# Performance work log

Hardware: AMD Instinct MI355X
Metric: run time of the kernel (lower is better)

The kernel has to match this reference:

```python
import jax, jax.numpy as jnp
import numpy as np

B, N, E, D, H, C, U = 512, 256, 1024, 256, 256, 8, 64
MARGIN_T, RISK_T, SCALE = 0.2, 0.6, 0.1
NEG = -1.0e9


def setup_inputs() -> dict:
    key = jax.random.key(0)
    ks = jax.random.split(key, 30)
    s = 0.02
    inp = dict(
        features=jax.random.normal(ks[0], (B, D), jnp.float32),
        centered_scores=jax.random.normal(ks[1], (B, N), jnp.float32),
        margin=jax.random.uniform(ks[2], (B,), jnp.float32),
        boundary_risk=jax.random.uniform(ks[3], (B,), jnp.float32),
        edge_sensitivity=jax.random.normal(ks[4], (B, E), jnp.float32),
        coords=jax.random.normal(ks[5], (B, N, C), jnp.float32),
        uncertainty=jax.random.uniform(ks[6], (B, U), jnp.float32),
        Wc1=jax.random.normal(ks[7], (D, H), jnp.float32) * s,
        bc1=jnp.zeros((H,), jnp.float32),
        Wc2=jax.random.normal(ks[8], (H, H), jnp.float32) * s,
        bc2=jnp.zeros((H,), jnp.float32),
        Wn1=jax.random.normal(ks[9], (H + C + 2, H), jnp.float32) * s,
        bn1=jnp.zeros((H,), jnp.float32),
        Wn2=jax.random.normal(ks[10], (H, 1), jnp.float32) * s,
        bn2=jnp.zeros((1,), jnp.float32),
        We1=jax.random.normal(ks[11], (H + C + 2, H), jnp.float32) * s,
        be1=jnp.zeros((H,), jnp.float32),
        We2=jax.random.normal(ks[12], (H, 1), jnp.float32) * s,
        be2=jnp.zeros((1,), jnp.float32),
        Wg=jax.random.normal(ks[13], (H, 1), jnp.float32) * s,
        bg=jnp.zeros((1,), jnp.float32),
        action_mask=jax.random.bernoulli(ks[14], 0.8, (B, N)),
        edge_mask=jax.random.bernoulli(ks[15], 0.8, (B, E)),
        actions=jax.random.randint(ks[16], (B, N), 0, U, jnp.int32),
        edges=jax.random.randint(ks[17], (B, E, 2), 0, N, jnp.int32),
    )
    return inp


def _mlp2(x, W1, b1, W2, b2):
    return jax.nn.relu(x @ W1 + b1) @ W2 + b2


def reference(features, centered_scores, margin, boundary_risk, edge_sensitivity,
              coords, uncertainty, Wc1, bc1, Wc2, bc2, Wn1, bn1, Wn2, bn2,
              We1, be1, We2, be2, Wg, bg, action_mask, edge_mask, actions, edges):
    amf = action_mask.astype(jnp.float32)
    emf = edge_mask.astype(jnp.float32)

    # context MLP
    h = jax.nn.relu(jax.nn.relu(features @ Wc1 + bc1) @ Wc2 + bc2)  # [B,H]

    low_margin = (margin < MARGIN_T).astype(jnp.float32)
    high_risk = (boundary_risk > RISK_T).astype(jnp.float32)
    learned_gate = jax.nn.sigmoid((h @ Wg + bg)[:, 0])
    refine_gate = jnp.maximum(jnp.maximum(low_margin, high_risk),
                              (learned_gate > 0.5).astype(jnp.float32))  # [B]

    # node features: [B,N,H+C+2]
    act = jnp.clip(actions, 0, U - 1)
    unc_g = jnp.take_along_axis(uncertainty, act, axis=1)  # [B,N]
    h_n = jnp.broadcast_to(h[:, None, :], (B, N, H))
    node_feats = jnp.concatenate(
        [h_n, coords, centered_scores[..., None], unc_g[..., None]], axis=-1)
    node_delta = _mlp2(node_feats, Wn1, bn1, Wn2, bn2)[..., 0] * amf  # [B,N]

    # edge features: gather src/dst coords
    e = jnp.clip(edges, 0, N - 1)
    src_c = jnp.take_along_axis(coords, e[:, :, 0:1], axis=1)  # [B,E,C]
    dst_c = jnp.take_along_axis(coords, e[:, :, 1:2], axis=1)  # [B,E,C]
    h_e = jnp.broadcast_to(h[:, None, :], (B, E, H))
    edge_feats = jnp.concatenate(
        [h_e, dst_c - src_c, edge_sensitivity[..., None], emf[..., None]], axis=-1)
    edge_delta = _mlp2(edge_feats, We1, be1, We2, be2)[..., 0] * emf  # [B,E]

    gate_node = refine_gate[:, None]
    refined_scores = (centered_scores + gate_node * SCALE * node_delta) * amf
    denom = jnp.clip(amf.sum(-1, keepdims=True), 1.0, None)  # [B,1]
    refined_scores = (refined_scores - refined_scores.sum(-1, keepdims=True) / denom) * amf

    refined_edge = (edge_sensitivity + gate_node * SCALE * edge_delta) * emf

    masked_top = jnp.where(action_mask, refined_scores, NEG)
    top_vals, top_idx = jax.lax.top_k(masked_top, 2)
    refined_margin = top_vals[:, 0] - top_vals[:, 1]

    # masked per-batch variance of refined_edge (biased), 0 if <=1 valid entry
    cnt = emf.sum(-1)
    cnt_c = jnp.clip(cnt, 1.0, None)
    mean = (refined_edge * emf).sum(-1) / cnt_c
    var = (emf * (refined_edge - mean[:, None]) ** 2).sum(-1) / cnt_c
    edge_var = jnp.where(cnt > 1.0, var, 0.0)

    unc_term = (unc_g * amf).sum(-1) / denom[:, 0]
    refined_risk = jnp.clip(
        jax.nn.sigmoid(-refined_margin) + 0.2 * edge_var + 0.1 * unc_term, 0.0, 1.0)

    return (refined_scores, refined_margin, refined_edge,
            top_idx[:, 0], refined_risk, refine_gate)
```

## Files before the change

### kernel.cpp

```cpp
#include <hip/hip_runtime.h>
#include <math.h>

#define B 512
#define N 256
#define E 1024
#define D 256
#define H 256
#define C 8
#define U 64

__device__ __forceinline__ float mask_val(const void* m, long i, int flag) {
    if (flag == 1) return ((const unsigned char*)m)[i] ? 1.f : 0.f;
    if (flag == 2) return (((const float*)m)[i] != 0.f) ? 1.f : 0.f;
    return ((const int*)m)[i] ? 1.f : 0.f;
}

__device__ __forceinline__ float block_sum(float v, float* red) {
    int t = threadIdx.x;
    red[t] = v; __syncthreads();
    for (int s = 128; s > 0; s >>= 1) {
        if (t < s) red[t] += red[t + s];
        __syncthreads();
    }
    float r = red[0]; __syncthreads();
    return r;
}

__global__ __launch_bounds__(512) void k_h(
    const float* __restrict__ feat,
    const float* __restrict__ Wc1, const float* __restrict__ bc1,
    const float* __restrict__ Wc2, const float* __restrict__ bc2,
    const float* __restrict__ Wn1, const float* __restrict__ bn1,
    const float* __restrict__ We1, const float* __restrict__ be1,
    const float* __restrict__ Wg,  const float* __restrict__ bg,
    const float* __restrict__ margin, const float* __restrict__ brisk,
    const unsigned int* __restrict__ amask_words,
    float* __restrict__ base_n, float* __restrict__ base_e,
    float* __restrict__ out_gate, int* __restrict__ flag)
{
    __shared__ __align__(16) float sF[2][256];
    __shared__ __align__(16) float sH[2][256];
    __shared__ float red[512];
    __shared__ int cls0, cls1;

    int t = threadIdx.x;
    int w = t >> 8;
    int c = t & 255;
    int b0 = blockIdx.x * 2;
    int b = b0 + w;

    if (blockIdx.x == 0) {
        if (t == 0) { cls0 = 0; cls1 = 0; }
        __syncthreads();
        if (t < 256) {
            unsigned int wd = amask_words[t];
            if (wd != 0u && wd != 1u) {
                if (wd == 0x3f800000u) atomicOr(&cls1, 1);
                else                   atomicOr(&cls0, 1);
            }
        }
        __syncthreads();
        if (t == 0) *flag = cls0 ? 1 : (cls1 ? 2 : 0);
    }

    sF[w][c] = feat[(long)b * D + c];
    __syncthreads();

    {
        float acc[4] = {bc1[c], 0.f, 0.f, 0.f};
        const float* Wp = Wc1 + c;
        for (int d0 = 0; d0 < D; d0 += 16) {
            float wv[16];
            #pragma unroll
            for (int k = 0; k < 16; k++) wv[k] = Wp[(long)(d0 + k) * H];
            #pragma unroll
            for (int k = 0; k < 16; k++)
                acc[k & 3] = fmaf(sF[w][d0 + k], wv[k], acc[k & 3]);
        }
        sH[w][c] = fmaxf((acc[0] + acc[1]) + (acc[2] + acc[3]), 0.f);
    }
    __syncthreads();

    {
        float acc[4] = {bc2[c], 0.f, 0.f, 0.f};
        const float* Wp = Wc2 + c;
        for (int d0 = 0; d0 < H; d0 += 16) {
            float wv[16];
            #pragma unroll
            for (int k = 0; k < 16; k++) wv[k] = Wp[(long)(d0 + k) * H];
            #pragma unroll
            for (int k = 0; k < 16; k++)
                acc[k & 3] = fmaf(sH[w][d0 + k], wv[k], acc[k & 3]);
        }
        float a = fmaxf((acc[0] + acc[1]) + (acc[2] + acc[3]), 0.f);
        __syncthreads();
        sF[w][c] = a;
    }
    __syncthreads();

    red[t] = sF[w][c] * Wg[c];
    __syncthreads();
    for (int s = 128; s > 0; s >>= 1) {
        if (c < s) red[t] += red[t + s];
        __syncthreads();
    }
    if (c == 0) {
        float lg = 1.f / (1.f + expf(-(red[t] + bg[0])));
        out_gate[b] = ((margin[b] < 0.2f) || (brisk[b] > 0.6f) || (lg > 0.5f)) ? 1.f : 0.f;
    }

    {
        const float* W3  = w ? (We1 + c) : (Wn1 + c);
        float bias       = w ? be1[c]    : bn1[c];
        float* dst       = w ? base_e    : base_n;
        float aA[2] = {bias, 0.f};
        float aB[2] = {bias, 0.f};
        for (int d0 = 0; d0 < H; d0 += 16) {
            float wv[16];
            #pragma unroll
            for (int k = 0; k < 16; k++) wv[k] = W3[(long)(d0 + k) * H];
            #pragma unroll
            for (int k = 0; k < 16; k++) {
                aA[k & 1] = fmaf(sF[0][d0 + k], wv[k], aA[k & 1]);
                aB[k & 1] = fmaf(sF[1][d0 + k], wv[k], aB[k & 1]);
            }
        }
        dst[(long)b0 * H + c]       = aA[0] + aA[1];
        dst[(long)(b0 + 1) * H + c] = aB[0] + aB[1];
    }
}

__global__ __launch_bounds__(256) void k_ne(
    const float* __restrict__ cs, const float* __restrict__ coords,
    const float* __restrict__ unc, const int* __restrict__ actions,
    const void* __restrict__ amask,
    const float* __restrict__ Wn1, const float* __restrict__ Wn2,
    const float* __restrict__ bn2, const float* __restrict__ base_n,
    const float* __restrict__ es, const int* __restrict__ edges,
    const void* __restrict__ emask,
    const float* __restrict__ We1, const float* __restrict__ We2,
    const float* __restrict__ be2, const float* __restrict__ base_e,
    const float* __restrict__ gate, const int* __restrict__ flagp,
    float* __restrict__ out0, float* __restrict__ out1, float* __restrict__ out2,
    float* __restrict__ out3, float* __restrict__ riskbase, float* __restrict__ evar)
{
    __shared__ __align__(16) float smem[4096 + 2048];
    float* pack = smem;
    int t = threadIdx.x;
    int flag = *flagp;

    if (blockIdx.x < 512) {
        int b = blockIdx.x;
        float g = gate[b];
        float am = mask_val(amask, (long)b * N + t, flag);
        float csv = cs[(long)b * N + t];
        int a = actions[(long)b * N + t];
        a = min(max(a, 0), U - 1);
        float ug = unc[(long)b * U + a];

        float raw;
        if (g != 0.f) {
            #pragma unroll
            for (int i = 0; i < 4; i++) {
                int lin = t + 256 * i;
                int j = lin >> 2, kq = (lin & 3) * 4;
                float4 v;
                if (kq == 0)
                    v = make_float4(Wn1[(long)(H+0)*H+j], Wn1[(long)(H+1)*H+j],
                                    Wn1[(long)(H+2)*H+j], Wn1[(long)(H+3)*H+j]);
                else if (kq == 4)
                    v = make_float4(Wn1[(long)(H+4)*H+j], Wn1[(long)(H+5)*H+j],
                                    Wn1[(long)(H+6)*H+j], Wn1[(long)(H+7)*H+j]);
                else if (kq == 8)
                    v = make_float4(Wn1[(long)(H+8)*H+j], Wn1[(long)(H+9)*H+j],
                                    Wn2[j], base_n[(long)b*H+j]);
                else
                    v = make_float4(0.f, 0.f, 0.f, 0.f);
                ((float4*)pack)[lin] = v;
            }

            const float4* cp = (const float4*)(coords + ((long)b * N + t) * C);
            float4 c0 = cp[0], c1 = cp[1];
            float f0 = c0.x, f1 = c0.y, f2 = c0.z, f3 = c0.w;
            float f4 = c1.x, f5 = c1.y, f6 = c1.z, f7 = c1.w;
            float f8 = csv, f9 = ug;
            float acc = bn2[0];
            __syncthreads();

            const float4* pk = (const float4*)pack;
            #pragma unroll 2
            for (int j = 0; j < H; j++) {
                float4 wa = pk[j*4+0];
                float4 wb = pk[j*4+1];
                float4 wc = pk[j*4+2];
                float zA = fmaf(f0, wa.x, wc.w);
                zA = fmaf(f1, wa.y, zA);
                zA = fmaf(f2, wa.z, zA);
                zA = fmaf(f3, wa.w, zA);
                float zB = f4 * wb.x;
                zB = fmaf(f5, wb.y, zB);
                zB = fmaf(f6, wb.z, zB);
                zB = fmaf(f7, wb.w, zB);
                zB = fmaf(f8, wc.x, zB);
                zB = fmaf(f9, wc.y, zB);
                acc = fmaf(fmaxf(zA + zB, 0.f), wc.z, acc);
            }
            raw = (csv + g * 0.1f * (acc * am)) * am;
            __syncthreads();
        } else {
            raw = csv * am;
        }

        float* red = smem + 4096;
        int* ridx = (int*)(smem + 4096 + 256);

        float sum = block_sum(raw, red);
        float cnt = block_sum(am, red);
        float denom = fmaxf(cnt, 1.f);
        float rs = (raw - sum / denom) * am;
        out0[(long)b * N + t] = rs;

        float masked = (am != 0.f) ? rs : -1e9f;

        red[t] = masked; ridx[t] = t; __syncthreads();
        for (int s = 128; s > 0; s >>= 1) {
            if (t < s) {
                float o = red[t + s]; int oi = ridx[t + s];
                if (o > red[t] || (o == red[t] && oi < ridx[t])) { red[t] = o; ridx[t] = oi; }
            }
            __syncthreads();
        }
        float v1 = red[0]; int i1 = ridx[0]; __syncthreads();

        red[t] = (t == i1) ? -1e9f : masked; __syncthreads();
        for (int s = 128; s > 0; s >>= 1) {
            if (t < s) red[t] = fmaxf(red[t], red[t + s]);
            __syncthreads();
        }
        float v2 = red[0]; __syncthreads();
        float rmargin = v1 - v2;

        float su = block_sum(ug * am, red);

        if (t == 0) {
            out1[b] = rmargin;
            out3[b] = (float)i1;
            float sig = 1.f / (1.f + expf(rmargin));
            riskbase[b] = sig + 0.1f * (su / denom);
        }
    } else {
        int b = blockIdx.x - 512;
        float g = gate[b];
        float (*sC)[8] = (float (*)[8])(smem + 4096);

        float re[4], emv[4];
        if (g != 0.f) {
            {
                float4* sc4 = (float4*)&sC[0][0];
                const float4* g4 = (const float4*)(coords + (long)b * N * C);
                sc4[t] = g4[t];
                sc4[t + 256] = g4[t + 256];
            }
            #pragma unroll
            for (int i = 0; i < 4; i++) {
                int lin = t + 256 * i;
                int j = lin >> 2, kq = (lin & 3) * 4;
                float4 v;
                if (kq == 0)
                    v = make_float4(We1[(long)(H+0)*H+j], We1[(long)(H+1)*H+j],
                                    We1[(long)(H+2)*H+j], We1[(long)(H+3)*H+j]);
                else if (kq == 4)
                    v = make_float4(We1[(long)(H+4)*H+j], We1[(long)(H+5)*H+j],
                                    We1[(long)(H+6)*H+j], We1[(long)(H+7)*H+j]);
                else if (kq == 8)
                    v = make_float4(We1[(long)(H+8)*H+j], We2[j],
                                    base_e[(long)b*H+j] + We1[(long)(H+9)*H+j], 0.f);
                else
                    v = make_float4(0.f, 0.f, 0.f, 0.f);
                ((float4*)pack)[lin] = v;
            }
            float b2v = be2[0];
            __syncthreads();

            float f[4][9], acc[4];
            #pragma unroll
            for (int q = 0; q < 4; q++) {
                int e = t + 256 * q;
                int2 ev = ((const int2*)edges)[(long)b * E + e];
                int s0 = min(max(ev.x, 0), N - 1);
                int d0 = min(max(ev.y, 0), N - 1);
                #pragma unroll
                for (int k = 0; k < 8; k++) f[q][k] = sC[d0][k] - sC[s0][k];
                f[q][8] = es[(long)b * E + e];
                emv[q] = mask_val(emask, (long)b * E + e, flag);
                acc[q] = b2v;
            }

            const float4* pk = (const float4*)pack;
            #pragma unroll 2
            for (int j = 0; j < H; j++) {
                float4 wa = pk[j*4+0];
                float4 wb = pk[j*4+1];
                float4 wc = pk[j*4+2];
                #pragma unroll
                for (int q = 0; q < 4; q++) {
                    float zA = fmaf(f[q][0], wa.x, wc.z);
                    zA = fmaf(f[q][1], wa.y, zA);
                    zA = fmaf(f[q][2], wa.z, zA);
                    zA = fmaf(f[q][3], wa.w, zA);
                    float zB = f[q][4] * wb.x;
                    zB = fmaf(f[q][5], wb.y, zB);
                    zB = fmaf(f[q][6], wb.z, zB);
                    zB = fmaf(f[q][7], wb.w, zB);
                    zB = fmaf(f[q][8], wc.x, zB);
                    acc[q] = fmaf(fmaxf(zA + zB, 0.f), wc.y, acc[q]);
                }
            }

            #pragma unroll
            for (int q = 0; q < 4; q++) {
                re[q] = (emv[q] != 0.f) ? (f[q][8] + g * 0.1f * acc[q]) : 0.f;
                out2[(long)b * E + t + 256 * q] = re[q];
            }
        } else {
            #pragma unroll
            for (int q = 0; q < 4; q++) {
                int e = t + 256 * q;
                emv[q] = mask_val(emask, (long)b * E + e, flag);
                re[q] = es[(long)b * E + e] * emv[q];
                out2[(long)b * E + e] = re[q];
            }
        }

        __syncthreads();
        float* red = smem + 4096;

        float S1 = 0.f, ce = 0.f;
        #pragma unroll
        for (int q = 0; q < 4; q++) { S1 += re[q]; ce += emv[q]; }
        float S1t = block_sum(S1, red);
        float cet = block_sum(ce, red);
        float mean = S1t / fmaxf(cet, 1.f);
        float v = 0.f;
        #pragma unroll
        for (int q = 0; q < 4; q++) {
            float dd = re[q] - mean;
            v = fmaf(emv[q] * dd, dd, v);
        }
        float vt = block_sum(v, red);
        if (t == 0) {
            float var = vt / fmaxf(cet, 1.f);
            evar[b] = (cet > 1.f) ? var : 0.f;
        }
    }
}

__global__ __launch_bounds__(256) void k_risk(
    const float* __restrict__ riskbase, const float* __restrict__ evar,
    float* __restrict__ out4)
{
    int b = blockIdx.x * 256 + threadIdx.x;
    float r = riskbase[b] + 0.2f * evar[b];
    out4[b] = fminf(fmaxf(r, 0.f), 1.f);
}

extern "C" void kernel_launch(void* const* d_in, const int* in_sizes, int n_in,
                              void* d_out, int out_size, void* d_ws, size_t ws_size,
                              hipStream_t stream) {
    const float* feat   = (const float*)d_in[0];
    const float* cs     = (const float*)d_in[1];
    const float* marg   = (const float*)d_in[2];
    const float* brisk  = (const float*)d_in[3];
    const float* es     = (const float*)d_in[4];
    const float* coords = (const float*)d_in[5];
    const float* unc    = (const float*)d_in[6];
    const float* Wc1    = (const float*)d_in[7];
    const float* bc1    = (const float*)d_in[8];
    const float* Wc2    = (const float*)d_in[9];
    const float* bc2    = (const float*)d_in[10];
    const float* Wn1    = (const float*)d_in[11];
    const float* bn1    = (const float*)d_in[12];
    const float* Wn2    = (const float*)d_in[13];
    const float* bn2    = (const float*)d_in[14];
    const float* We1    = (const float*)d_in[15];
    const float* be1    = (const float*)d_in[16];
    const float* We2    = (const float*)d_in[17];
    const float* be2    = (const float*)d_in[18];
    const float* Wg     = (const float*)d_in[19];
    const float* bg     = (const float*)d_in[20];
    const void*  amask  = d_in[21];
    const void*  emask  = d_in[22];
    const int*   actions= (const int*)d_in[23];
    const int*   edges  = (const int*)d_in[24];

    float* out0 = (float*)d_out;
    float* out1 = out0 + (long)B * N;
    float* out2 = out1 + B;
    float* out3 = out2 + (long)B * E;
    float* out4 = out3 + B;
    float* out5 = out4 + B;

    float* base_n  = (float*)d_ws;
    float* base_e  = base_n + (long)B * H;
    float* riskbase= base_e + (long)B * H;
    float* evar    = riskbase + B;
    int*   flag    = (int*)(evar + B);

    k_h<<<B / 2, 512, 0, stream>>>(feat, Wc1, bc1, Wc2, bc2, Wn1, bn1, We1, be1,
                                   Wg, bg, marg, brisk,
                                   (const unsigned int*)amask,
                                   base_n, base_e, out5, flag);
    k_ne<<<1024, 256, 0, stream>>>(cs, coords, unc, actions, amask,
                                   Wn1, Wn2, bn2, base_n,
                                   es, edges, emask,
                                   We1, We2, be2, base_e,
                                   out5, flag,
                                   out0, out1, out2, out3, riskbase, evar);
    k_risk<<<2, 256, 0, stream>>>(riskbase, evar, out4);
}
```

Measured before the change: 80.80 us.

## Split node/edge hidden dim across blocks with atomic accumulation and separate finalize kernel

The node and edge MLP second layers are split across four hidden-dimension quarters per batch. Partial sums are accumulated with atomicAdd into zeroed buffers, with zeroing done inside k_h. Node blocks now process four batches each with 64 hidden units, and a new k_fin kernel applies masks, biases, normalization, top-2 and variance. The goal is more parallel blocks and shorter per-block loops for better occupancy, at the cost of atomics, an extra kernel launch and an extra round trip of intermediates through global memory.

```diff
diff --git a/kernel.cpp b/kernel.cpp
--- a/kernel.cpp
+++ b/kernel.cpp
@@ -8,6 +8,9 @@
 #define H 256
 #define C 8
 #define U 64
+
+#define NODE_GRID 512
+#define EDGE_GRID 2048
 
 __device__ __forceinline__ float mask_val(const void* m, long i, int flag) {
     if (flag == 1) return ((const unsigned char*)m)[i] ? 1.f : 0.f;
@@ -36,7 +39,8 @@
     const float* __restrict__ margin, const float* __restrict__ brisk,
     const unsigned int* __restrict__ amask_words,
     float* __restrict__ base_n, float* __restrict__ base_e,
-    float* __restrict__ out_gate, int* __restrict__ flag)
+    float* __restrict__ out_gate, int* __restrict__ flag,
+    float* __restrict__ node_delta, float* __restrict__ out2)
 {
     __shared__ __align__(16) float sF[2][256];
     __shared__ __align__(16) float sH[2][256];
@@ -48,6 +52,12 @@
     int c = t & 255;
     int b0 = blockIdx.x * 2;
     int b = b0 + w;
+
+    {
+        int idx = blockIdx.x * 512 + t;
+        node_delta[idx] = 0.f;
+        ((float4*)out2)[idx] = make_float4(0.f, 0.f, 0.f, 0.f);
+    }
 
     if (blockIdx.x == 0) {
         if (t == 0) { cls0 = 0; cls1 = 0; }
@@ -133,23 +143,175 @@
 __global__ __launch_bounds__(256) void k_ne(
     const float* __restrict__ cs, const float* __restrict__ coords,
     const float* __restrict__ unc, const int* __restrict__ actions,
-    const void* __restrict__ amask,
     const float* __restrict__ Wn1, const float* __restrict__ Wn2,
-    const float* __restrict__ bn2, const float* __restrict__ base_n,
+    const float* __restrict__ base_n,
     const float* __restrict__ es, const int* __restrict__ edges,
-    const void* __restrict__ emask,
     const float* __restrict__ We1, const float* __restrict__ We2,
-    const float* __restrict__ be2, const float* __restrict__ base_e,
+    const float* __restrict__ base_e,
+    const float* __restrict__ gate,
+    float* __restrict__ node_delta, float* __restrict__ out2)
+{
+    __shared__ __align__(16) float smem[2816];
+    int t = threadIdx.x;
+
+    if (blockIdx.x < NODE_GRID) {
+        int rg = blockIdx.x >> 2;
+        int jq = blockIdx.x & 3;
+        int b0 = rg * 4;
+        float* sB   = smem;
+        float* pack = smem + 256;
+
+        {
+            int i = t;
+            #pragma unroll
+            for (int s = 0; s < 3; s++, i += 256) {
+                int j = i / 12, k = i - j * 12;
+                int jj = jq * 64 + j;
+                float v;
+                if (k < 10)      v = Wn1[(long)(H + k) * H + jj];
+                else if (k == 10) v = Wn2[jj];
+                else             v = 0.f;
+                pack[i] = v;
+            }
+            int r = t >> 6, j = t & 63;
+            sB[r * 64 + j] = base_n[(long)(b0 + r) * H + jq * 64 + j];
+        }
+        __syncthreads();
+
+        int w = t >> 6, lane = t & 63;
+        int b = b0 + w;
+        float g = gate[b];
+        if (g == 0.f) return;
+
+        float f[4][10], acc[4];
+        #pragma unroll
+        for (int q = 0; q < 4; q++) {
+            int n = q * 64 + lane;
+            const float4* cp = (const float4*)(coords + ((long)b * N + n) * C);
+            float4 c0 = cp[0], c1 = cp[1];
+            f[q][0] = c0.x; f[q][1] = c0.y; f[q][2] = c0.z; f[q][3] = c0.w;
+            f[q][4] = c1.x; f[q][5] = c1.y; f[q][6] = c1.z; f[q][7] = c1.w;
+            f[q][8] = cs[(long)b * N + n];
+            int a = actions[(long)b * N + n];
+            a = min(max(a, 0), U - 1);
+            f[q][9] = unc[(long)b * U + a];
+            acc[q] = 0.f;
+        }
+
+        const float4* pk = (const float4*)pack;
+        const float* sBw = sB + w * 64;
+        #pragma unroll 4
+        for (int j = 0; j < 64; j++) {
+            float4 wa = pk[j * 3 + 0];
+            float4 wb = pk[j * 3 + 1];
+            float4 wc = pk[j * 3 + 2];
+            float bse = sBw[j];
+            #pragma unroll
+            for (int q = 0; q < 4; q++) {
+                float zA = fmaf(f[q][0], wa.x, bse);
+                zA = fmaf(f[q][1], wa.y, zA);
+                zA = fmaf(f[q][2], wa.z, zA);
+                zA = fmaf(f[q][3], wa.w, zA);
+                float zB = f[q][4] * wb.x;
+                zB = fmaf(f[q][5], wb.y, zB);
+                zB = fmaf(f[q][6], wb.z, zB);
+                zB = fmaf(f[q][7], wb.w, zB);
+                zB = fmaf(f[q][8], wc.x, zB);
+                zB = fmaf(f[q][9], wc.y, zB);
+                acc[q] = fmaf(fmaxf(zA + zB, 0.f), wc.z, acc[q]);
+            }
+        }
+
+        #pragma unroll
+        for (int q = 0; q < 4; q++)
+            atomicAdd(&node_delta[(long)b * N + q * 64 + lane], acc[q]);
+    } else {
+        int eb = blockIdx.x - NODE_GRID;
+        int b = eb >> 2, jq = eb & 3;
+        float g = gate[b];
+        if (g == 0.f) return;
+
+        float (*sC)[8] = (float (*)[8])smem;
+        float* pack = smem + 2048;
+
+        {
+            float4* sc4 = (float4*)smem;
+            const float4* g4 = (const float4*)(coords + (long)b * N * C);
+            sc4[t] = g4[t];
+            sc4[t + 256] = g4[t + 256];
+            int i = t;
+            #pragma unroll
+            for (int s = 0; s < 3; s++, i += 256) {
+                int j = i / 12, k = i - j * 12;
+                int jj = jq * 64 + j;
+                float v;
+                if (k < 9)        v = We1[(long)(H + k) * H + jj];
+                else if (k == 9)  v = We2[jj];
+                else if (k == 10) v = base_e[(long)b * H + jj]
+                                      + We1[(long)(H + 9) * H + jj];
+                else              v = 0.f;
+                pack[i] = v;
+            }
+        }
+        __syncthreads();
+
+        float f[4][9], acc[4];
+        #pragma unroll
+        for (int q = 0; q < 4; q++) {
+            int e = t + 256 * q;
+            int2 ev = ((const int2*)edges)[(long)b * E + e];
+            int s0 = min(max(ev.x, 0), N - 1);
+            int d0 = min(max(ev.y, 0), N - 1);
+            #pragma unroll
+            for (int k = 0; k < 8; k++) f[q][k] = sC[d0][k] - sC[s0][k];
+            f[q][8] = es[(long)b * E + e];
+            acc[q] = 0.f;
+        }
+
+        const float4* pk = (const float4*)pack;
+        #pragma unroll 4
+        for (int j = 0; j < 64; j++) {
+            float4 wa = pk[j * 3 + 0];
+            float4 wb = pk[j * 3 + 1];
+            float4 wc = pk[j * 3 + 2];
+            #pragma unroll
+            for (int q = 0; q < 4; q++) {
+                float zA = fmaf(f[q][0], wa.x, wc.z);
+                zA = fmaf(f[q][1], wa.y, zA);
+                zA = fmaf(f[q][2], wa.z, zA);
+                zA = fmaf(f[q][3], wa.w, zA);
+                float zB = f[q][4] * wb.x;
+                zB = fmaf(f[q][5], wb.y, zB);
+                zB = fmaf(f[q][6], wb.z, zB);
+                zB = fmaf(f[q][7], wb.w, zB);
+                zB = fmaf(f[q][8], wc.x, zB);
+                acc[q] = fmaf(fmaxf(zA + zB, 0.f), wc.y, acc[q]);
+            }
+        }
+
+        #pragma unroll
+        for (int q = 0; q < 4; q++)
+            atomicAdd(&out2[(long)b * E + t + 256 * q], acc[q]);
+    }
+}
+
+__global__ __launch_bounds__(256) void k_fin(
+    const void* __restrict__ amask, const void* __restrict__ emask,
+    const int* __restrict__ actions, const float* __restrict__ unc,
+    const float* __restrict__ cs, const float* __restrict__ es,
+    const float* __restrict__ bn2, const float* __restrict__ be2,
     const float* __restrict__ gate, const int* __restrict__ flagp,
-    float* __restrict__ out0, float* __restrict__ out1, float* __restrict__ out2,
-    float* __restrict__ out3, float* __restrict__ riskbase, float* __restrict__ evar)
+    const float* __restrict__ node_delta,
+    float* __restrict__ out0, float* __restrict__ out1,
+    float* __restrict__ out2, float* __restrict__ out3,
+    float* __restrict__ riskbase, float* __restrict__ evar)
 {
-    __shared__ __align__(16) float smem[4096 + 2048];
-    float* pack = smem;
+    __shared__ float red[256];
+    __shared__ int ridx[256];
     int t = threadIdx.x;
     int flag = *flagp;
 
-    if (blockIdx.x < 512) {
+    if (blockIdx.x < B) {
         int b = blockIdx.x;
         float g = gate[b];
         float am = mask_val(amask, (long)b * N + t, flag);
@@ -157,62 +319,8 @@
         int a = actions[(long)b * N + t];
         a = min(max(a, 0), U - 1);
         float ug = unc[(long)b * U + a];
-
-        float raw;
-        if (g != 0.f) {
-            #pragma unroll
-            for (int i = 0; i < 4; i++) {
-                int lin = t + 256 * i;
-                int j = lin >> 2, kq = (lin & 3) * 4;
-                float4 v;
-                if (kq == 0)
-                    v = make_float4(Wn1[(long)(H+0)*H+j], Wn1[(long)(H+1)*H+j],
-                                    Wn1[(long)(H+2)*H+j], Wn1[(long)(H+3)*H+j]);
-                else if (kq == 4)
-                    v = make_float4(Wn1[(long)(H+4)*H+j], Wn1[(long)(H+5)*H+j],
-                                    Wn1[(long)(H+6)*H+j], Wn1[(long)(H+7)*H+j]);
-                else if (kq == 8)
-                    v = make_float4(Wn1[(long)(H+8)*H+j], Wn1[(long)(H+9)*H+j],
-                                    Wn2[j], base_n[(long)b*H+j]);
-                else
-                    v = make_float4(0.f, 0.f, 0.f, 0.f);
-                ((float4*)pack)[lin] = v;
-            }
-
-            const float4* cp = (const float4*)(coords + ((long)b * N + t) * C);
-            float4 c0 = cp[0], c1 = cp[1];
-            float f0 = c0.x, f1 = c0.y, f2 = c0.z, f3 = c0.w;
-            float f4 = c1.x, f5 = c1.y, f6 = c1.z, f7 = c1.w;
-            float f8 = csv, f9 = ug;
-            float acc = bn2[0];
-            __syncthreads();
-
-            const float4* pk = (const float4*)pack;
-            #pragma unroll 2
-            for (int j = 0; j < H; j++) {
-                float4 wa = pk[j*4+0];
-                float4 wb = pk[j*4+1];
-                float4 wc = pk[j*4+2];
-                float zA = fmaf(f0, wa.x, wc.w);
-                zA = fmaf(f1, wa.y, zA);
-                zA = fmaf(f2, wa.z, zA);
-                zA = fmaf(f3, wa.w, zA);
-                float zB = f4 * wb.x;
-                zB = fmaf(f5, wb.y, zB);
-                zB = fmaf(f6, wb.z, zB);
-                zB = fmaf(f7, wb.w, zB);
-                zB = fmaf(f8, wc.x, zB);
-                zB = fmaf(f9, wc.y, zB);
-                acc = fmaf(fmaxf(zA + zB, 0.f), wc.z, acc);
-            }
-            raw = (csv + g * 0.1f * (acc * am)) * am;
-            __syncthreads();
-        } else {
-            raw = csv * am;
-        }
-
-        float* red = smem + 4096;
-        int* ridx = (int*)(smem + 4096 + 256);
+        float nd = (node_delta[(long)b * N + t] + bn2[0]) * am;
+        float raw = (csv + g * 0.1f * nd) * am;
 
         float sum = block_sum(raw, red);
         float cnt = block_sum(am, red);
@@ -249,91 +357,20 @@
             riskbase[b] = sig + 0.1f * (su / denom);
         }
     } else {
-        int b = blockIdx.x - 512;
+        int b = blockIdx.x - B;
         float g = gate[b];
-        float (*sC)[8] = (float (*)[8])(smem + 4096);
+        float be2v = be2[0];
 
         float re[4], emv[4];
-        if (g != 0.f) {
-            {
-                float4* sc4 = (float4*)&sC[0][0];
-                const float4* g4 = (const float4*)(coords + (long)b * N * C);
-                sc4[t] = g4[t];
-                sc4[t + 256] = g4[t + 256];
-            }
-            #pragma unroll
-            for (int i = 0; i < 4; i++) {
-                int lin = t + 256 * i;
-                int j = lin >> 2, kq = (lin & 3) * 4;
-                float4 v;
-                if (kq == 0)
-                    v = make_float4(We1[(long)(H+0)*H+j], We1[(long)(H+1)*H+j],
-                                    We1[(long)(H+2)*H+j], We1[(long)(H+3)*H+j]);
-                else if (kq == 4)
-                    v = make_float4(We1[(long)(H+4)*H+j], We1[(long)(H+5)*H+j],
-                                    We1[(long)(H+6)*H+j], We1[(long)(H+7)*H+j]);
-                else if (kq == 8)
-                    v = make_float4(We1[(long)(H+8)*H+j], We2[j],
-                                    base_e[(long)b*H+j] + We1[(long)(H+9)*H+j], 0.f);
-                else
-                    v = make_float4(0.f, 0.f, 0.f, 0.f);
-                ((float4*)pack)[lin] = v;
-            }
-            float b2v = be2[0];
-            __syncthreads();
-
-            float f[4][9], acc[4];
-            #pragma unroll
-            for (int q = 0; q < 4; q++) {
-                int e = t + 256 * q;
-                int2 ev = ((const int2*)edges)[(long)b * E + e];
-                int s0 = min(max(ev.x, 0), N - 1);
-                int d0 = min(max(ev.y, 0), N - 1);
-                #pragma unroll
-                for (int k = 0; k < 8; k++) f[q][k] = sC[d0][k] - sC[s0][k];
-                f[q][8] = es[(long)b * E + e];
-                emv[q] = mask_val(emask, (long)b * E + e, flag);
-                acc[q] = b2v;
-            }
-
-            const float4* pk = (const float4*)pack;
-            #pragma unroll 2
-            for (int j = 0; j < H; j++) {
-                float4 wa = pk[j*4+0];
-                float4 wb = pk[j*4+1];
-                float4 wc = pk[j*4+2];
-                #pragma unroll
-                for (int q = 0; q < 4; q++) {
-                    float zA = fmaf(f[q][0], wa.x, wc.z);
-                    zA = fmaf(f[q][1], wa.y, zA);
-                    zA = fmaf(f[q][2], wa.z, zA);
-                    zA = fmaf(f[q][3], wa.w, zA);
-                    float zB = f[q][4] * wb.x;
-                    zB = fmaf(f[q][5], wb.y, zB);
-                    zB = fmaf(f[q][6], wb.z, zB);
-                    zB = fmaf(f[q][7], wb.w, zB);
-                    zB = fmaf(f[q][8], wc.x, zB);
-                    acc[q] = fmaf(fmaxf(zA + zB, 0.f), wc.y, acc[q]);
-                }
-            }
-
-            #pragma unroll
-            for (int q = 0; q < 4; q++) {
-                re[q] = (emv[q] != 0.f) ? (f[q][8] + g * 0.1f * acc[q]) : 0.f;
-                out2[(long)b * E + t + 256 * q] = re[q];
-            }
-        } else {
-            #pragma unroll
-            for (int q = 0; q < 4; q++) {
-                int e = t + 256 * q;
-                emv[q] = mask_val(emask, (long)b * E + e, flag);
-                re[q] = es[(long)b * E + e] * emv[q];
-                out2[(long)b * E + e] = re[q];
-            }
-        }
-
-        __syncthreads();
-        float* red = smem + 4096;
+        #pragma unroll
+        for (int q = 0; q < 4; q++) {
+            long idx = (long)b * E + t + 256 * q;
+            emv[q] = mask_val(emask, idx, flag);
+            float delta = out2[idx] + be2v;
+            float r = es[idx] + g * 0.1f * delta;
+            re[q] = (emv[q] != 0.f) ? r : 0.f;
+            out2[idx] = re[q];
+        }
 
         float S1 = 0.f, ce = 0.f;
         #pragma unroll
@@ -400,21 +437,26 @@
     float* out4 = out3 + B;
     float* out5 = out4 + B;
 
-    float* base_n  = (float*)d_ws;
-    float* base_e  = base_n + (long)B * H;
-    float* riskbase= base_e + (long)B * H;
-    float* evar    = riskbase + B;
-    int*   flag    = (int*)(evar + B);
+    float* base_n     = (float*)d_ws;
+    float* base_e     = base_n + (long)B * H;
+    float* node_delta = base_e + (long)B * H;
+    float* riskbase   = node_delta + (long)B * N;
+    float* evar       = riskbase + B;
+    int*   flag       = (int*)(evar + B);
 
     k_h<<<B / 2, 512, 0, stream>>>(feat, Wc1, bc1, Wc2, bc2, Wn1, bn1, We1, be1,
                                    Wg, bg, marg, brisk,
                                    (const unsigned int*)amask,
-                                   base_n, base_e, out5, flag);
-    k_ne<<<1024, 256, 0, stream>>>(cs, coords, unc, actions, amask,
-                                   Wn1, Wn2, bn2, base_n,
-                                   es, edges, emask,
-                                   We1, We2, be2, base_e,
-                                   out5, flag,
-                                   out0, out1, out2, out3, riskbase, evar);
+                                   base_n, base_e, out5, flag,
+                                   node_delta, out2);
+    k_ne<<<NODE_GRID + EDGE_GRID, 256, 0, stream>>>(
+        cs, coords, unc, actions,
+        Wn1, Wn2, base_n,
+        es, edges,
+        We1, We2, base_e,
+        out5, node_delta, out2);
+    k_fin<<<2 * B, 256, 0, stream>>>(amask, emask, actions, unc, cs, es,
+                                     bn2, be2, out5, flag, node_delta,
+                                     out0, out1, out2, out3, riskbase, evar);
     k_risk<<<2, 256, 0, stream>>>(riskbase, evar, out4);
 }
```

After: 80.43 us. Within noise of the previous version (-0.5%).

## Split edge MLP across two blocks per batch and move variance to separate kernel

Applied to the files above, without the earlier changes.

Each batch's edge work now runs on two blocks of 512 edges instead of one block of 1024, so the grid grows to 1536 blocks and is better balanced against the node blocks. Because a batch's edges are no longer in one block, the masked variance reduction moves into a new k_fin kernel that re-reads out2 from global memory, which costs an extra launch and an extra pass over the data. Weight packing into shared memory changes to a 12-float stride filled with coalesced per-thread loads. Coordinates are now stored with a 9-float stride, likely to reduce LDS bank conflicts on the gathered reads.

```diff
diff --git a/kernel.cpp b/kernel.cpp
--- a/kernel.cpp
+++ b/kernel.cpp
@@ -141,15 +141,16 @@
     const float* __restrict__ We1, const float* __restrict__ We2,
     const float* __restrict__ be2, const float* __restrict__ base_e,
     const float* __restrict__ gate, const int* __restrict__ flagp,
-    float* __restrict__ out0, float* __restrict__ out1, float* __restrict__ out2,
-    float* __restrict__ out3, float* __restrict__ riskbase, float* __restrict__ evar)
+    float* __restrict__ out0, float* __restrict__ out1,
+    float* __restrict__ out2, float* __restrict__ out3,
+    float* __restrict__ riskbase)
 {
-    __shared__ __align__(16) float smem[4096 + 2048];
+    __shared__ __align__(16) float smem[3072 + 2304];
     float* pack = smem;
     int t = threadIdx.x;
     int flag = *flagp;
 
-    if (blockIdx.x < 512) {
+    if (blockIdx.x < B) {
         int b = blockIdx.x;
         float g = gate[b];
         float am = mask_val(amask, (long)b * N + t, flag);
@@ -160,25 +161,13 @@
 
         float raw;
         if (g != 0.f) {
-            #pragma unroll
-            for (int i = 0; i < 4; i++) {
-                int lin = t + 256 * i;
-                int j = lin >> 2, kq = (lin & 3) * 4;
-                float4 v;
-                if (kq == 0)
-                    v = make_float4(Wn1[(long)(H+0)*H+j], Wn1[(long)(H+1)*H+j],
-                                    Wn1[(long)(H+2)*H+j], Wn1[(long)(H+3)*H+j]);
-                else if (kq == 4)
-                    v = make_float4(Wn1[(long)(H+4)*H+j], Wn1[(long)(H+5)*H+j],
-                                    Wn1[(long)(H+6)*H+j], Wn1[(long)(H+7)*H+j]);
-                else if (kq == 8)
-                    v = make_float4(Wn1[(long)(H+8)*H+j], Wn1[(long)(H+9)*H+j],
-                                    Wn2[j], base_n[(long)b*H+j]);
-                else
-                    v = make_float4(0.f, 0.f, 0.f, 0.f);
-                ((float4*)pack)[lin] = v;
-            }
-
+            {
+                float* p = pack + t * 12;
+                #pragma unroll
+                for (int k = 0; k < 10; k++) p[k] = Wn1[(long)(H + k) * H + t];
+                p[10] = Wn2[t];
+                p[11] = base_n[(long)b * H + t];
+            }
             const float4* cp = (const float4*)(coords + ((long)b * N + t) * C);
             float4 c0 = cp[0], c1 = cp[1];
             float f0 = c0.x, f1 = c0.y, f2 = c0.z, f3 = c0.w;
@@ -187,12 +176,12 @@
             float acc = bn2[0];
             __syncthreads();
 
-            const float4* pk = (const float4*)pack;
-            #pragma unroll 2
+            #pragma unroll 4
             for (int j = 0; j < H; j++) {
-                float4 wa = pk[j*4+0];
-                float4 wb = pk[j*4+1];
-                float4 wc = pk[j*4+2];
+                const float* pj = pack + j * 12;
+                float4 wa = *(const float4*)(pj);
+                float4 wb = *(const float4*)(pj + 4);
+                float4 wc = *(const float4*)(pj + 8);
                 float zA = fmaf(f0, wa.x, wc.w);
                 zA = fmaf(f1, wa.y, zA);
                 zA = fmaf(f2, wa.z, zA);
@@ -211,8 +200,8 @@
             raw = csv * am;
         }
 
-        float* red = smem + 4096;
-        int* ridx = (int*)(smem + 4096 + 256);
+        float* red = smem + 3072;
+        int* ridx = (int*)(smem + 3072 + 256);
 
         float sum = block_sum(raw, red);
         float cnt = block_sum(am, red);
@@ -249,109 +238,117 @@
             riskbase[b] = sig + 0.1f * (su / denom);
         }
     } else {
-        int b = blockIdx.x - 512;
+        int eb = blockIdx.x - B;
+        int b = eb >> 1, half = eb & 1;
         float g = gate[b];
-        float (*sC)[8] = (float (*)[8])(smem + 4096);
-
-        float re[4], emv[4];
-        if (g != 0.f) {
-            {
-                float4* sc4 = (float4*)&sC[0][0];
-                const float4* g4 = (const float4*)(coords + (long)b * N * C);
-                sc4[t] = g4[t];
-                sc4[t + 256] = g4[t + 256];
-            }
-            #pragma unroll
-            for (int i = 0; i < 4; i++) {
-                int lin = t + 256 * i;
-                int j = lin >> 2, kq = (lin & 3) * 4;
-                float4 v;
-                if (kq == 0)
-                    v = make_float4(We1[(long)(H+0)*H+j], We1[(long)(H+1)*H+j],
-                                    We1[(long)(H+2)*H+j], We1[(long)(H+3)*H+j]);
-                else if (kq == 4)
-                    v = make_float4(We1[(long)(H+4)*H+j], We1[(long)(H+5)*H+j],
-                                    We1[(long)(H+6)*H+j], We1[(long)(H+7)*H+j]);
-                else if (kq == 8)
-                    v = make_float4(We1[(long)(H+8)*H+j], We2[j],
-                                    base_e[(long)b*H+j] + We1[(long)(H+9)*H+j], 0.f);
-                else
-                    v = make_float4(0.f, 0.f, 0.f, 0.f);
-                ((float4*)pack)[lin] = v;
-            }
-            float b2v = be2[0];
-            __syncthreads();
-
-            float f[4][9], acc[4];
-            #pragma unroll
-            for (int q = 0; q < 4; q++) {
-                int e = t + 256 * q;
-                int2 ev = ((const int2*)edges)[(long)b * E + e];
-                int s0 = min(max(ev.x, 0), N - 1);
-                int d0 = min(max(ev.y, 0), N - 1);
-                #pragma unroll
-                for (int k = 0; k < 8; k++) f[q][k] = sC[d0][k] - sC[s0][k];
-                f[q][8] = es[(long)b * E + e];
-                emv[q] = mask_val(emask, (long)b * E + e, flag);
-                acc[q] = b2v;
-            }
-
-            const float4* pk = (const float4*)pack;
-            #pragma unroll 2
-            for (int j = 0; j < H; j++) {
-                float4 wa = pk[j*4+0];
-                float4 wb = pk[j*4+1];
-                float4 wc = pk[j*4+2];
-                #pragma unroll
-                for (int q = 0; q < 4; q++) {
-                    float zA = fmaf(f[q][0], wa.x, wc.z);
-                    zA = fmaf(f[q][1], wa.y, zA);
-                    zA = fmaf(f[q][2], wa.z, zA);
-                    zA = fmaf(f[q][3], wa.w, zA);
-                    float zB = f[q][4] * wb.x;
-                    zB = fmaf(f[q][5], wb.y, zB);
-                    zB = fmaf(f[q][6], wb.z, zB);
-                    zB = fmaf(f[q][7], wb.w, zB);
-                    zB = fmaf(f[q][8], wc.x, zB);
-                    acc[q] = fmaf(fmaxf(zA + zB, 0.f), wc.y, acc[q]);
-                }
-            }
-
-            #pragma unroll
-            for (int q = 0; q < 4; q++) {
-                re[q] = (emv[q] != 0.f) ? (f[q][8] + g * 0.1f * acc[q]) : 0.f;
-                out2[(long)b * E + t + 256 * q] = re[q];
-            }
-        } else {
-            #pragma unroll
-            for (int q = 0; q < 4; q++) {
-                int e = t + 256 * q;
-                emv[q] = mask_val(emask, (long)b * E + e, flag);
-                re[q] = es[(long)b * E + e] * emv[q];
-                out2[(long)b * E + e] = re[q];
-            }
-        }
-
-        __syncthreads();
-        float* red = smem + 4096;
-
-        float S1 = 0.f, ce = 0.f;
+        int e0 = half * 512 + t;
+
+        if (g == 0.f) {
+            #pragma unroll
+            for (int q = 0; q < 2; q++) {
+                long idx = (long)b * E + e0 + 256 * q;
+                float em = mask_val(emask, idx, flag);
+                out2[idx] = es[idx] * em;
+            }
+            return;
+        }
+
+        float* sC = smem + 3072;
+
+        {
+            const float4* g4 = (const float4*)(coords + (long)b * N * C);
+            float4 c0 = g4[t * 2], c1 = g4[t * 2 + 1];
+            float* dst = sC + t * 9;
+            dst[0] = c0.x; dst[1] = c0.y; dst[2] = c0.z; dst[3] = c0.w;
+            dst[4] = c1.x; dst[5] = c1.y; dst[6] = c1.z; dst[7] = c1.w;
+        }
+        {
+            float* p = pack + t * 12;
+            #pragma unroll
+            for (int k = 0; k < 9; k++) p[k] = We1[(long)(H + k) * H + t];
+            p[9] = We2[t];
+            p[10] = base_e[(long)b * H + t] + We1[(long)(H + 9) * H + t];
+            p[11] = 0.f;
+        }
+        float b2v = be2[0];
+        __syncthreads();
+
+        float f[2][9], acc[2], emv[2];
         #pragma unroll
-        for (int q = 0; q < 4; q++) { S1 += re[q]; ce += emv[q]; }
-        float S1t = block_sum(S1, red);
-        float cet = block_sum(ce, red);
-        float mean = S1t / fmaxf(cet, 1.f);
-        float v = 0.f;
+        for (int q = 0; q < 2; q++) {
+            long idx = (long)b * E + e0 + 256 * q;
+            int2 ev = ((const int2*)edges)[idx];
+            int s0 = min(max(ev.x, 0), N - 1);
+            int d0 = min(max(ev.y, 0), N - 1);
+            const float* cs0 = sC + s0 * 9;
+            const float* cd0 = sC + d0 * 9;
+            #pragma unroll
+            for (int k = 0; k < 8; k++) f[q][k] = cd0[k] - cs0[k];
+            f[q][8] = es[idx];
+            emv[q] = mask_val(emask, idx, flag);
+            acc[q] = b2v;
+        }
+
+        #pragma unroll 4
+        for (int j = 0; j < H; j++) {
+            const float* pj = pack + j * 12;
+            float4 wa = *(const float4*)(pj);
+            float4 wb = *(const float4*)(pj + 4);
+            float4 wc = *(const float4*)(pj + 8);
+            #pragma unroll
+            for (int q = 0; q < 2; q++) {
+                float zA = fmaf(f[q][0], wa.x, wc.z);
+                zA = fmaf(f[q][1], wa.y, zA);
+                zA = fmaf(f[q][2], wa.z, zA);
+                zA = fmaf(f[q][3], wa.w, zA);
+                float zB = f[q][4] * wb.x;
+                zB = fmaf(f[q][5], wb.y, zB);
+                zB = fmaf(f[q][6], wb.z, zB);
+                zB = fmaf(f[q][7], wb.w, zB);
+                zB = fmaf(f[q][8], wc.x, zB);
+                acc[q] = fmaf(fmaxf(zA + zB, 0.f), wc.y, acc[q]);
+            }
+        }
+
         #pragma unroll
-        for (int q = 0; q < 4; q++) {
-            float dd = re[q] - mean;
-            v = fmaf(emv[q] * dd, dd, v);
-        }
-        float vt = block_sum(v, red);
-        if (t == 0) {
-            float var = vt / fmaxf(cet, 1.f);
-            evar[b] = (cet > 1.f) ? var : 0.f;
-        }
+        for (int q = 0; q < 2; q++) {
+            long idx = (long)b * E + e0 + 256 * q;
+            out2[idx] = (emv[q] != 0.f) ? (f[q][8] + g * 0.1f * acc[q]) : 0.f;
+        }
+    }
+}
+
+__global__ __launch_bounds__(256) void k_fin(
+    const void* __restrict__ emask, const int* __restrict__ flagp,
+    const float* __restrict__ out2, float* __restrict__ evar)
+{
+    __shared__ float red[256];
+    int t = threadIdx.x;
+    int b = blockIdx.x;
+    int flag = *flagp;
+
+    float x[4], em[4];
+    float S1 = 0.f, ce = 0.f;
+    #pragma unroll
+    for (int q = 0; q < 4; q++) {
+        long idx = (long)b * E + t + 256 * q;
+        x[q] = out2[idx];
+        em[q] = mask_val(emask, idx, flag);
+        S1 += x[q]; ce += em[q];
+    }
+    float S1t = block_sum(S1, red);
+    float cet = block_sum(ce, red);
+    float mean = S1t / fmaxf(cet, 1.f);
+    float v = 0.f;
+    #pragma unroll
+    for (int q = 0; q < 4; q++) {
+        float dd = x[q] - mean;
+        v = fmaf(em[q] * dd, dd, v);
+    }
+    float vt = block_sum(v, red);
+    if (t == 0) {
+        float var = vt / fmaxf(cet, 1.f);
+        evar[b] = (cet > 1.f) ? var : 0.f;
     }
 }
 
@@ -400,21 +397,22 @@
     float* out4 = out3 + B;
     float* out5 = out4 + B;
 
-    float* base_n  = (float*)d_ws;
-    float* base_e  = base_n + (long)B * H;
-    float* riskbase= base_e + (long)B * H;
-    float* evar    = riskbase + B;
-    int*   flag    = (int*)(evar + B);
+    float* base_n   = (float*)d_ws;
+    float* base_e   = base_n + (long)B * H;
+    float* riskbase = base_e + (long)B * H;
+    float* evar     = riskbase + B;
+    int*   flag     = (int*)(evar + B);
 
     k_h<<<B / 2, 512, 0, stream>>>(feat, Wc1, bc1, Wc2, bc2, Wn1, bn1, We1, be1,
                                    Wg, bg, marg, brisk,
                                    (const unsigned int*)amask,
                                    base_n, base_e, out5, flag);
-    k_ne<<<1024, 256, 0, stream>>>(cs, coords, unc, actions, amask,
-                                   Wn1, Wn2, bn2, base_n,
-                                   es, edges, emask,
-                                   We1, We2, be2, base_e,
-                                   out5, flag,
-                                   out0, out1, out2, out3, riskbase, evar);
+    k_ne<<<B + 2 * B, 256, 0, stream>>>(cs, coords, unc, actions, amask,
+                                        Wn1, Wn2, bn2, base_n,
+                                        es, edges, emask,
+                                        We1, We2, be2, base_e,
+                                        out5, flag,
+                                        out0, out1, out2, out3, riskbase);
+    k_fin<<<B, 256, 0, stream>>>(emask, flag, out2, evar);
     k_risk<<<2, 256, 0, stream>>>(riskbase, evar, out4);
 }
```

New measurement: 87.73 us. 8.6% more time.
